# Optimization experiments

Hardware: AMD Instinct MI355X
Metric: run time of the kernel (lower is better)

Reference implementation:

```python
import jax, jax.numpy as jnp
import numpy as np
import math

HIDDEN = 768
HEADS = 12
HEAD_DIM = HIDDEN // HEADS
BLOCK = 256
TOPK = 3
BATCH = 2
SEQ = 2048


def setup_inputs() -> dict:
    key = jax.random.key(0)
    ks = jax.random.split(key, 5)
    s = 1.0 / math.sqrt(HIDDEN)
    return {
        "hidden_states": jax.random.normal(ks[0], (BATCH, SEQ, HIDDEN), jnp.float32),
        "Wq": jax.random.normal(ks[1], (HIDDEN, HIDDEN), jnp.float32) * s,
        "Wk": jax.random.normal(ks[2], (HIDDEN, HIDDEN), jnp.float32) * s,
        "Wv": jax.random.normal(ks[3], (HIDDEN, HIDDEN), jnp.float32) * s,
        "Wo": jax.random.normal(ks[4], (HIDDEN, HIDDEN), jnp.float32) * s,
    }


def _rope(x, sin, cos):
    # x: [B, H, S, D]; rotate-half RoPE
    d2 = x.shape[-1] // 2
    x1, x2 = x[..., :d2], x[..., d2:]
    return x * cos + jnp.concatenate([-x2, x1], axis=-1) * sin


def reference(hidden_states, Wq, Wk, Wv, Wo):
    B, S, Hd = hidden_states.shape
    H, D, bs, K = HEADS, HEAD_DIM, BLOCK, TOPK
    nb = S // bs  # number of key blocks
    scale = 1.0 / math.sqrt(D)

    def split_heads(x):
        return x.reshape(B, S, H, D).transpose(0, 2, 1, 3)  # [B,H,S,D]

    q = split_heads(hidden_states @ Wq.T)
    k = split_heads(hidden_states @ Wk.T)
    v = split_heads(hidden_states @ Wv.T)

    # rotary embedding (standard rotate-half RoPE, base 10000)
    inv_freq = 1.0 / (10000.0 ** (jnp.arange(0, D, 2, dtype=jnp.float32) / D))
    ang = jnp.arange(S, dtype=jnp.float32)[:, None] * inv_freq[None, :]  # [S, D/2]
    emb = jnp.concatenate([ang, ang], axis=-1)  # [S, D]
    sin, cos = jnp.sin(emb), jnp.cos(emb)
    q = _rope(q, sin, cos)
    k = _rope(k, sin, cos)

    # mean-pooled block representations of keys: [B,H,nb,D]
    block_reps = k.reshape(B, H, nb, bs, D).mean(axis=3)

    # routing scores: per-token score against each block rep
    bscores = jnp.einsum('bhsd,bhnd->bhsn', q, block_reps) * scale  # [B,H,S,nb]
    pos = jnp.arange(S)
    cur = pos // bs                       # current block of each query, [S]
    blk = jnp.arange(nb)
    future = blk[None, None, None, :] > cur[None, None, :, None]
    bscores = jnp.where(future, -jnp.inf, bscores)
    # current block is force-selected (score set to dtype max)
    is_cur = blk[None, None, None, :] == cur[None, None, :, None]
    bscores = jnp.where(is_cur, jnp.finfo(bscores.dtype).max, bscores)

    _, topk_idx = jax.lax.top_k(bscores, min(K, nb))  # [B,H,S,K]
    selected = jnp.sum(jax.nn.one_hot(topk_idx, nb, dtype=jnp.float32), axis=-2) > 0  # [B,H,S,nb]

    # per-key-position mask: key t allowed iff its block is selected for query i,
    # and within the current block only t <= i (matches original truncation).
    sel_t = selected[:, :, :, cur]                          # [B,H,Sq,Sk]
    intra_ok = (cur[None, :] != cur[:, None]) | (pos[None, :] <= pos[:, None])  # [Sq,Sk]
    mask = sel_t & intra_ok[None, None]

    scores = jnp.einsum('bhqd,bhkd->bhqk', q, k) * scale
    scores = jnp.where(mask, scores, -jnp.inf)
    probs = jax.nn.softmax(scores, axis=-1)
    out = jnp.einsum('bhqk,bhkd->bhqd', probs, v)

    out = out.transpose(0, 2, 1, 3).reshape(B, S, Hd)
    return out @ Wo.T
```

## Files before the change

kernel.cpp:

```cpp
#include <hip/hip_runtime.h>
#include <math.h>


#define HID   768
#define NH    12
#define DH    64
#define SEQN  2048
#define BATCH 2
#define NTOK  (BATCH*SEQN)
#define NB    8
#define BLKSZ 256
#define NEG_INF (-__builtin_huge_valf())
#define POS_INF (__builtin_huge_valf())
#define LO_SCALE 2048.0f
#define LO_INV   (1.0f/2048.0f)
#define EXP2C    0.18033688f

#define SPLIT_ROWS 1024
#define NBH   (BATCH*NH)

typedef unsigned short u16;
typedef _Float16 v8hf __attribute__((ext_vector_type(8)));
typedef float    v4f  __attribute__((ext_vector_type(4)));

__device__ __forceinline__ u16 f2h(float x) {
    _Float16 h = (_Float16)x;
    return __builtin_bit_cast(u16, h);
}
__device__ __forceinline__ float h2f(u16 u) {
    return (float)__builtin_bit_cast(_Float16, u);
}
__device__ __forceinline__ v8hf ldhf8(const u16* p) {
    return *reinterpret_cast<const v8hf*>(p);
}
__device__ __forceinline__ void g2lds16(const u16* g, u16* l) {
    __builtin_amdgcn_global_load_lds(
        (const __attribute__((address_space(1))) void*)g,
        (__attribute__((address_space(3))) void*)l, 16, 0, 0);
}
#define MFMA16(a, b, c) __builtin_amdgcn_mfma_f32_16x16x32_f16(a, b, c, 0, 0, 0)

__device__ const int g_uord[48] = {
    46,47,44,45,15,
    42,43,40,41,14,
    38,39,36,37,13,
    34,35,32,33,12,
    30,31,28,29,11,
    26,27,24,25,10,
    22,23,20,21, 9,
    18,19,16,17, 8,
     7, 6, 5, 4, 3, 2, 1, 0
};

__global__ __launch_bounds__(256)
void preproc_k(const float* __restrict__ X,  const float* __restrict__ Wq,
               const float* __restrict__ Wk, const float* __restrict__ Wv,
               const float* __restrict__ Wo, float2* __restrict__ tab,
               u16* __restrict__ Xh, u16* __restrict__ Xl,
               u16* __restrict__ Wq2, u16* __restrict__ Wk2,
               u16* __restrict__ Wv2, u16* __restrict__ Wo2)
{
    const int NW = HID * HID;
    const int id = blockIdx.x;
    const int tid = threadIdx.x;
    if (id < 12288) {
        const int i = id * 256 + tid;
        const float x = X[i];
        const u16 h = f2h(x);
        Xh[i] = h;
        Xl[i] = f2h((x - h2f(h)) * LO_SCALE);
    } else if (id < 21504) {
        const int j = (id - 12288) * 256 + tid;
        const int z = j / NW, i = j - z * NW;
        const float* src = (z == 0) ? Wq : (z == 1) ? Wk : (z == 2) ? Wv : Wo;
        u16* dst = (z == 0) ? Wq2 : (z == 1) ? Wk2 : (z == 2) ? Wv2 : Wo2;
        const float x = src[i];
        const u16 h = f2h(x);
        dst[i] = h;
        dst[i + NW] = f2h((x - h2f(h)) * LO_SCALE);
    } else {
        const int i = (id - 21504) * 256 + tid;
        const int s = i >> 5, f = i & 31;
        const double y  = exp((double)f * (log(10000.0) / 32.0));
        const float yf = (float)y;
        const float invf = 1.0f / yf;
        const float ang  = (float)s * invf;
        tab[i] = make_float2((float)sin((double)ang), (float)cos((double)ang));
    }
}

__device__ __forceinline__
void qkv_mainloop(const u16* __restrict__ Ah, const u16* __restrict__ Al,
                  const u16* __restrict__ Bh, const u16* __restrict__ Bl,
                  int m0, int nb0, bool hasC0,
                  u16* As, u16* Bs, v4f acc01[2][4], v4f acc2[2][4])
{
    const int tid = threadIdx.x;
    const int w = tid >> 6, lane = tid & 63;
    const int col = lane & 15, quad = lane >> 4;
    const int AOFF = 128 * 64, BOFF = 64 * 64;

    int a_row[4], a_gl[4];
    #pragma unroll
    for (int r = 0; r < 4; r++) {
        const int g = r * 256 + tid;
        a_row[r] = g >> 3;
        a_gl[r]  = (g & 7) ^ (a_row[r] & 7);
    }
    int b_row[2], b_gl[2];
    #pragma unroll
    for (int r = 0; r < 2; r++) {
        const int g = r * 256 + tid;
        b_row[r] = g >> 3;
        b_gl[r]  = (g & 7) ^ (b_row[r] & 7);
    }

    for (int itc = 0; itc < HID / 64; itc++) {
        const int k0 = itc * 64;
        __syncthreads();
        #pragma unroll
        for (int r = 0; r < 4; r++)
            g2lds16(Ah + (size_t)(m0 + a_row[r]) * HID + k0 + a_gl[r] * 8,
                    &As[(r * 256 + w * 64) * 8]);
        if (hasC0) {
            #pragma unroll
            for (int r = 0; r < 4; r++)
                g2lds16(Al + (size_t)(m0 + a_row[r]) * HID + k0 + a_gl[r] * 8,
                        &As[AOFF + (r * 256 + w * 64) * 8]);
        }
        #pragma unroll
        for (int r = 0; r < 2; r++) {
            g2lds16(Bh + (size_t)(nb0 + b_row[r]) * HID + k0 + b_gl[r] * 8,
                    &Bs[(r * 256 + w * 64) * 8]);
            g2lds16(Bl + (size_t)(nb0 + b_row[r]) * HID + k0 + b_gl[r] * 8,
                    &Bs[BOFF + (r * 256 + w * 64) * 8]);
        }
        __syncthreads();
        #pragma unroll
        for (int ks = 0; ks < 2; ks++) {
            v8hf afh[2], afl[2], bfh[4], bfl[4];
            #pragma unroll
            for (int mt = 0; mt < 2; mt++) {
                const int row = w * 32 + mt * 16 + col;
                const int gph = (ks * 4 + quad) ^ (row & 7);
                afh[mt] = ldhf8(&As[row * 64 + gph * 8]);
                if (hasC0) afl[mt] = ldhf8(&As[AOFF + row * 64 + gph * 8]);
            }
            #pragma unroll
            for (int nt = 0; nt < 4; nt++) {
                const int row = nt * 16 + col;
                const int gph = (ks * 4 + quad) ^ (row & 7);
                bfh[nt] = ldhf8(&Bs[row * 64 + gph * 8]);
                bfl[nt] = ldhf8(&Bs[BOFF + row * 64 + gph * 8]);
            }
            #pragma unroll
            for (int mt = 0; mt < 2; mt++)
                #pragma unroll
                for (int nt = 0; nt < 4; nt++) {
                    if (hasC0)
                        acc01[mt][nt] = MFMA16(afl[mt], bfh[nt], acc01[mt][nt]);
                    acc01[mt][nt] = MFMA16(afh[mt], bfl[nt], acc01[mt][nt]);
                    acc2[mt][nt]  = MFMA16(afh[mt], bfh[nt], acc2[mt][nt]);
                }
        }
    }
    __syncthreads();
}

__global__ __launch_bounds__(256, 3)
void qkv_fused_gemm_k(const u16* __restrict__ Xh, const u16* __restrict__ Xl,
                      const u16* __restrict__ Wq2, const u16* __restrict__ Wk2,
                      const u16* __restrict__ Wv2, const float2* __restrict__ tab,
                      float* __restrict__ q32, u16* __restrict__ kh16,
                      u16* __restrict__ vth, float* __restrict__ partial)
{
    __shared__ u16 As[2 * 128 * 64];
    __shared__ u16 Bs[2 * 64 * 64];
    float (*psum)[64] = (float(*)[64])As;

    const int NW = HID * HID;
    const int id    = blockIdx.x;
    const int xcd   = id & 7, loc = id >> 3;
    const int mtile = xcd * 4 + (loc & 3);
    const int ntile = loc >> 2;
    const int m0  = mtile * 128;
    const int mat = ntile / 12;
    const int nb0 = (ntile - mat * 12) * 64;
    const u16* Bh = (mat == 0) ? Wq2 : (mat == 1) ? Wk2 : Wv2;

    v4f acc01[2][4] = {}, acc2[2][4] = {};
    qkv_mainloop(Xh, Xl, Bh, Bh + NW, m0, nb0, mat != 2, As, Bs, acc01, acc2);

    v4f acc[2][4];
    #pragma unroll
    for (int mt = 0; mt < 2; mt++)
        #pragma unroll
        for (int nt = 0; nt < 4; nt++)
            #pragma unroll
            for (int r = 0; r < 4; r++)
                acc[mt][nt][r] = acc01[mt][nt][r] * LO_INV + acc2[mt][nt][r];

    const int tid = threadIdx.x;
    const int w = tid >> 6, lane = tid & 63;
    const int col = lane & 15, quad = lane >> 4;
    const int b = m0 >> 11;
    const int h = nb0 >> 6;
    const size_t bh = (size_t)b * NH + h;

    if (mat == 2) {
        #pragma unroll
        for (int nt = 0; nt < 4; nt++) {
            const int d = nt * 16 + col;
            #pragma unroll
            for (int mt = 0; mt < 2; mt++) {
                const int m = m0 + w * 32 + mt * 16 + quad * 4;
                const int s = m & (SEQN - 1);
                ushort4 pk = make_ushort4(f2h(acc[mt][nt][0]), f2h(acc[mt][nt][1]),
                                          f2h(acc[mt][nt][2]), f2h(acc[mt][nt][3]));
                *(ushort4*)&vth[(bh * DH + d) * SEQN + s] = pk;
            }
        }
        return;
    }

    float vsum[4] = {0.f, 0.f, 0.f, 0.f};
    #pragma unroll
    for (int mt = 0; mt < 2; mt++) {
        #pragma unroll
        for (int nt = 0; nt < 4; nt++) {
            const int d = nt * 16 + col;
            #pragma unroll
            for (int r = 0; r < 4; r++) {
                const int m = m0 + w * 32 + mt * 16 + quad * 4 + r;
                const int s = m & (SEQN - 1);
                const float part = acc[mt][nt ^ 2][r];
                const float2 sc = tab[(s << 5) + (d & 31)];
                const float val = (d < 32) ? acc[mt][nt][r] * sc.y - part * sc.x
                                           : acc[mt][nt][r] * sc.y + part * sc.x;
                const size_t idx = (bh * SEQN + s) * DH + d;
                if (mat == 0) {
                    q32[idx] = val;
                } else {
                    kh16[idx] = f2h(val);
                    vsum[nt] += val;
                }
            }
        }
    }
    if (mat == 1) {
        #pragma unroll
        for (int nt = 0; nt < 4; nt++) {
            float v = vsum[nt];
            v += __shfl_xor(v, 16);
            v += __shfl_xor(v, 32);
            if (quad == 0) psum[w][nt * 16 + col] = v;
        }
        __syncthreads();
        if (tid < 64) {
            const float s4 = (psum[0][tid] + psum[1][tid])
                           + (psum[2][tid] + psum[3][tid]);
            const int nblk = (m0 & (SEQN - 1)) >> 8;
            const int half = (m0 >> 7) & 1;
            partial[((bh * NB + nblk) * 2 + half) * 64 + tid] = s4;
        }
    }
}

__global__ __launch_bounds__(256, 3)
void out_gemm_mfma_k(const u16* __restrict__ Ah, const u16* __restrict__ Wo2,
                     float* __restrict__ C)
{
    __shared__ u16 As[64 * 64];
    __shared__ u16 Bs[2 * 64 * 64];
    const int BOFF = 64 * 64;

    const int NW = HID * HID;
    const int id    = blockIdx.x;
    const int xcd   = id & 7, loc = id >> 3;
    const int mtile = xcd * 8 + (loc & 7);
    const int ntile = loc >> 3;
    const int m0 = mtile * 64, n0 = ntile * 64;
    const int tid = threadIdx.x;
    const int w = tid >> 6, lane = tid & 63;
    const int col = lane & 15, quad = lane >> 4;

    const int r0 = tid >> 3,         gl0 = (tid & 7) ^ (r0 & 7);
    const int r1 = (256 + tid) >> 3, gl1 = ((256 + tid) & 7) ^ (r1 & 7);

    const u16* Bhp = Wo2;
    const u16* Blp = Wo2 + NW;

    v4f accL[4] = {}, accH[4] = {};
    for (int itc = 0; itc < HID / 64; itc++) {
        const int k0 = itc * 64;
        __syncthreads();
        g2lds16(Ah  + (size_t)(m0 + r0) * HID + k0 + gl0 * 8, &As[(w * 64) * 8]);
        g2lds16(Ah  + (size_t)(m0 + r1) * HID + k0 + gl1 * 8, &As[(256 + w * 64) * 8]);
        g2lds16(Bhp + (size_t)(n0 + r0) * HID + k0 + gl0 * 8, &Bs[(w * 64) * 8]);
        g2lds16(Bhp + (size_t)(n0 + r1) * HID + k0 + gl1 * 8, &Bs[(256 + w * 64) * 8]);
        g2lds16(Blp + (size_t)(n0 + r0) * HID + k0 + gl0 * 8, &Bs[BOFF + (w * 64) * 8]);
        g2lds16(Blp + (size_t)(n0 + r1) * HID + k0 + gl1 * 8, &Bs[BOFF + (256 + w * 64) * 8]);
        __syncthreads();
        #pragma unroll
        for (int ks = 0; ks < 2; ks++) {
            const int arow = w * 16 + col;
            v8hf a = ldhf8(&As[arow * 64 + (((ks * 4 + quad) ^ (arow & 7))) * 8]);
            #pragma unroll
            for (int nt = 0; nt < 4; nt++) {
                const int row = nt * 16 + col;
                const int g = (ks * 4 + quad) ^ (row & 7);
                accH[nt] = MFMA16(a, ldhf8(&Bs[row * 64 + g * 8]), accH[nt]);
                accL[nt] = MFMA16(a, ldhf8(&Bs[BOFF + row * 64 + g * 8]), accL[nt]);
            }
        }
    }

    #pragma unroll
    for (int nt = 0; nt < 4; nt++)
        #pragma unroll
        for (int r = 0; r < 4; r++) {
            const int m = m0 + w * 16 + quad * 4 + r;
            C[(size_t)m * HID + n0 + nt * 16 + col] =
                accL[nt][r] * LO_INV + accH[nt][r];
        }
}

__global__ __launch_bounds__(64)
void reps_reduce_k(const float* __restrict__ partial, float* __restrict__ reps)
{
    const int bhn = blockIdx.x;
    const int d = threadIdx.x;
    const float* p = &partial[(size_t)bhn * 128 + d];
    double s = (double)p[0] + (double)p[64];
    reps[(size_t)bhn * 64 + d] = (float)(s * (1.0 / 256.0));
}

__global__ __launch_bounds__(128)
void select_topk_k(const float* __restrict__ qg, const float* __restrict__ reps,
                   unsigned* __restrict__ selm)
{
    __shared__ float rs[NB][DH];
    const int bh = blockIdx.y;
    const int tid = threadIdx.x;
    for (int idx = tid; idx < NB * DH; idx += 128)
        rs[idx >> 6][idx & 63] = reps[(size_t)bh * NB * DH + idx];
    __syncthreads();

    const int qq = blockIdx.x * 128 + tid;
    const float* qv = &qg[((size_t)bh * SEQN + qq) * DH];
    float qr[DH];
    #pragma unroll
    for (int c = 0; c < 16; c++) {
        float4 t = *(const float4*)&qv[c * 4];
        qr[c*4+0]=t.x; qr[c*4+1]=t.y; qr[c*4+2]=t.z; qr[c*4+3]=t.w;
    }
    const int cur = qq >> 8;
    double sc[NB];
    #pragma unroll
    for (int n = 0; n < NB; n++) {
        double ssum = 0.0;
        for (int d = 0; d < DH; d++) ssum += (double)qr[d] * (double)rs[n][d];
        sc[n] = ssum * 0.125;
    }
    for (int n = cur + 1; n < NB; n++) sc[n] = -1e300;
    sc[cur] = 1e300;
    unsigned mask = 0;
    for (int p = 0; p < 3; p++) {
        int bi = -1; double bv = 0.0;
        for (int n = 0; n < NB; n++) {
            if ((mask >> n) & 1) continue;
            if (bi < 0 || sc[n] > bv) { bi = n; bv = sc[n]; }
        }
        mask |= 1u << bi;
    }
    selm[(size_t)bh * SEQN + qq] = mask;
}

__global__ __launch_bounds__(256, 4)
void moba_attn_k(const float* __restrict__ q32, const u16* __restrict__ kh16,
                 const u16* __restrict__ vth, const unsigned* __restrict__ selm,
                 u16* __restrict__ aoh, float* __restrict__ po,
                 float* __restrict__ ml)
{
    __shared__ u16 kbuf[2][64 * 64];
    __shared__ u16 vbuf[2][64 * 64];
    __shared__ u16 plds[4][16][64];
    unsigned* s_uni = (unsigned*)&vbuf[1][0];

    const int id  = blockIdx.x;
    const int xcd = id & 7, loc = id >> 3;
    const int bh  = xcd * 3 + loc / 48;
    const int u   = g_uord[loc % 48];
    int qb, split, stride;
    if (u < 16) { qb = u;                 split = 0;          stride = 1; }
    else        { qb = 16 + ((u - 16) >> 1); split = (u - 16) & 1; stride = 2; }
    const int q0  = qb * 64;
    const int cur = q0 >> 8;
    const int tid = threadIdx.x;
    const int wave = tid >> 6, lane = tid & 63;
    const int col = lane & 15, quad = lane >> 4;
    const int qw0 = q0 + wave * 16;
    const int qpos = qw0 + col;
    const size_t bhS = (size_t)bh * SEQN;
    const size_t bhV = (size_t)bh * DH;

    if (tid == 0) *s_uni = 0;
    __syncthreads();
    const unsigned mymask = selm[bhS + qw0 + col];
    unsigned uw = mymask;
    #pragma unroll
    for (int off = 1; off < 16; off <<= 1) uw |= __shfl_xor(uw, off);
    if (lane == 0) atomicOr(s_uni, uw);
    const unsigned wmask = __builtin_amdgcn_readfirstlane(uw);

    v8hf qh[2], ql[2];
    #pragma unroll
    for (int ks = 0; ks < 2; ks++) {
        const float* qp = &q32[(bhS + qw0 + col) * DH + ks * 32 + quad * 8];
        float4 f0 = *(const float4*)qp;
        float4 f1 = *(const float4*)(qp + 4);
        float qf[8] = {f0.x, f0.y, f0.z, f0.w, f1.x, f1.y, f1.z, f1.w};
        union { u16 u[8]; v8hf h; } uh, ul;
        #pragma unroll
        for (int j = 0; j < 8; j++) {
            u16 hb = f2h(qf[j]);
            uh.u[j] = hb;
            ul.u[j] = f2h((qf[j] - h2f(hb)) * LO_SCALE);
        }
        qh[ks] = uh.h; ql[ks] = ul.h;
    }
    __syncthreads();
    const unsigned uni = __builtin_amdgcn_readfirstlane(*s_uni);

    int n_nxt = __builtin_ctz(uni), c_nxt = 0;
    bool has_nxt = true;
    auto c2max = [&](int n) { return (n == cur) ? ((q0 + 63 - n * BLKSZ) >> 6) : 3; };
    auto advance1 = [&]() {
        if (c_nxt < c2max(n_nxt)) { c_nxt++; return; }
        for (int nn = n_nxt + 1; nn < NB; nn++)
            if ((uni >> nn) & 1) { n_nxt = nn; c_nxt = 0; return; }
        has_nxt = false;
    };
    for (int i = 0; i < split; i++) if (has_nxt) advance1();
    int n_cur = n_nxt, c_cur = c_nxt;
    const bool cur_valid = has_nxt;

    const size_t srow0 = (size_t)bh * SPLIT_ROWS + (q0 - SPLIT_ROWS);

    if (!cur_valid) {
        if (stride == 2) {
            if (quad == 0) {
                const size_t r = srow0 + wave * 16 + col;
                ml[(r * 2 + split) * 2 + 0] = NEG_INF;
                ml[(r * 2 + split) * 2 + 1] = 0.f;
            }
            #pragma unroll
            for (int nt = 0; nt < 4; nt++)
                #pragma unroll
                for (int r = 0; r < 4; r++) {
                    const size_t rq = srow0 + wave * 16 + quad * 4 + r;
                    po[(rq * 2 + split) * 64 + nt * 16 + col] = 0.f;
                }
        }
        return;
    }
    for (int i = 0; i < stride; i++) if (has_nxt) advance1();

    const int sg_row0 = tid >> 3;
    const int sg_gl0  = (tid & 7) ^ (sg_row0 & 7);
    const int sg_row1 = (256 + tid) >> 3;
    const int sg_gl1  = ((256 + tid) & 7) ^ (sg_row1 & 7);
    auto stage = [&](int n, int c2, int buf) {
        const int kb = n * BLKSZ + c2 * 64;
        u16* kd = (u16*)kbuf[buf];
        u16* vd = (u16*)vbuf[buf];
        const size_t ks0 = (bhS + kb + sg_row0) * DH + sg_gl0 * 8;
        const size_t ks1 = (bhS + kb + sg_row1) * DH + sg_gl1 * 8;
        const size_t vs0 = (bhV + sg_row0) * SEQN + kb + sg_gl0 * 8;
        const size_t vs1 = (bhV + sg_row1) * SEQN + kb + sg_gl1 * 8;
        g2lds16(kh16 + ks0, kd + (wave * 64) * 8);
        g2lds16(kh16 + ks1, kd + (256 + wave * 64) * 8);
        g2lds16(vth + vs0, vd + (wave * 64) * 8);
        g2lds16(vth + vs1, vd + (256 + wave * 64) * 8);
    };

    const v4f zero4 = {0.f, 0.f, 0.f, 0.f};
    v4f oacc[4] = {zero4, zero4, zero4, zero4};
    float m_i = NEG_INF, l_i = 0.f;
    const int psw = (col & 7) << 1;

    stage(n_cur, c_cur, 0);
    int t = 0;
    while (true) {
        __syncthreads();
        if (has_nxt) stage(n_nxt, c_nxt, (t + 1) & 1);

        const int n  = n_cur;
        const int kb = n * BLKSZ + c_cur * 64;
        const bool iscur = (n == cur);
        const float selinf = ((mymask >> n) & 1) ? 0.f : POS_INF;
        const bool need_mask = iscur && (kb + 63 > qw0);
        const u16* kd = (const u16*)kbuf[t & 1];
        const u16* vd = (const u16*)vbuf[t & 1];

        if ((wmask >> n) & 1) {
            v4f sf[4];
            __builtin_amdgcn_s_setprio(1);
            #pragma unroll
            for (int mt = 0; mt < 4; mt++) {
                const int row = mt * 16 + col;
                const int r7 = row & 7;
                v8hf kh0 = ldhf8(&kd[(row * 8 + (quad ^ r7)) * 8]);
                v8hf kh1 = ldhf8(&kd[(row * 8 + ((4 + quad) ^ r7)) * 8]);
                v4f c = zero4;
                c = MFMA16(kh0, ql[0], c);
                c = MFMA16(kh1, ql[1], c);
                #pragma unroll
                for (int r = 0; r < 4; r++) c[r] *= LO_INV;
                c = MFMA16(kh0, qh[0], c);
                c = MFMA16(kh1, qh[1], c);
                sf[mt] = c;
            }
            __builtin_amdgcn_s_setprio(0);

            if (need_mask) {
                #pragma unroll
                for (int mt = 0; mt < 4; mt++)
                    #pragma unroll
                    for (int r = 0; r < 4; r++) {
                        const int kidx = kb + mt * 16 + quad * 4 + r;
                        sf[mt][r] = (kidx <= qpos) ? sf[mt][r] : NEG_INF;
                    }
            }

            float rm = NEG_INF;
            #pragma unroll
            for (int mt = 0; mt < 4; mt++)
                #pragma unroll
                for (int r = 0; r < 4; r++) rm = fmaxf(rm, sf[mt][r]);
            rm = fmaxf(rm, __shfl_xor(rm, 16));
            rm = fmaxf(rm, __shfl_xor(rm, 32));
            rm = rm - selinf;
            const float mnew  = fmaxf(m_i, rm);
            const float alpha = (m_i == NEG_INF) ? 0.f : exp2f((m_i - mnew) * EXP2C);
            const float biasC = ((mnew == NEG_INF) ? 0.f : mnew * EXP2C) + selinf;

            float lsum = 0.f;
            #pragma unroll
            for (int mt = 0; mt < 4; mt++) {
                ushort4 hv;
                #pragma unroll
                for (int r = 0; r < 4; r++) {
                    float p = exp2f(fmaf(sf[mt][r], EXP2C, -biasC));
                    lsum += p;
                    u16 hu = f2h(p);
                    if (r == 0) hv.x = hu;
                    else if (r == 1) hv.y = hu;
                    else if (r == 2) hv.z = hu;
                    else hv.w = hu;
                }
                *(ushort4*)&plds[wave][col][((mt * 4 + quad) ^ psw) * 4] = hv;
            }
            lsum += __shfl_xor(lsum, 16);
            lsum += __shfl_xor(lsum, 32);
            l_i = l_i * alpha + lsum;
            m_i = mnew;

            float ar[4];
            #pragma unroll
            for (int r = 0; r < 4; r++) ar[r] = __shfl(alpha, quad * 4 + r, 16);
            #pragma unroll
            for (int nt = 0; nt < 4; nt++)
                #pragma unroll
                for (int r = 0; r < 4; r++) oacc[nt][r] *= ar[r];

            __threadfence_block();

            __builtin_amdgcn_s_setprio(1);
            #pragma unroll
            for (int ks2 = 0; ks2 < 2; ks2++) {
                v8hf ph = ldhf8(&plds[wave][col][((ks2 * 8 + quad * 2) ^ psw) * 4]);
                #pragma unroll
                for (int nt = 0; nt < 4; nt++) {
                    const int row = nt * 16 + col;
                    const int g = (ks2 * 4 + quad) ^ (row & 7);
                    v8hf vh = ldhf8(&vd[(row * 8 + g) * 8]);
                    oacc[nt] = MFMA16(ph, vh, oacc[nt]);
                }
            }
            __builtin_amdgcn_s_setprio(0);
        }

        if (!has_nxt) break;
        n_cur = n_nxt; c_cur = c_nxt;
        for (int i = 0; i < stride; i++) if (has_nxt) advance1();
        t++;
    }

    if (stride == 2) {
        if (quad == 0) {
            const size_t r = srow0 + wave * 16 + col;
            ml[(r * 2 + split) * 2 + 0] = m_i;
            ml[(r * 2 + split) * 2 + 1] = l_i;
        }
        #pragma unroll
        for (int nt = 0; nt < 4; nt++)
            #pragma unroll
            for (int r = 0; r < 4; r++) {
                const size_t rq = srow0 + wave * 16 + quad * 4 + r;
                po[(rq * 2 + split) * 64 + nt * 16 + col] = oacc[nt][r];
            }
        return;
    }

    const int b = bh / NH, h = bh % NH;
    const float invl = 1.f / l_i;
    float ir[4];
    #pragma unroll
    for (int r = 0; r < 4; r++) ir[r] = __shfl(invl, quad * 4 + r, 16);
    #pragma unroll
    for (int nt = 0; nt < 4; nt++)
        #pragma unroll
        for (int r = 0; r < 4; r++) {
            const int qi = qw0 + quad * 4 + r;
            const size_t idx = ((size_t)b * SEQN + qi) * HID + h * DH + nt * 16 + col;
            aoh[idx] = f2h(oacc[nt][r] * ir[r]);
        }
}

__global__ __launch_bounds__(256)
void attn_combine_k(const float* __restrict__ po, const float* __restrict__ ml,
                    u16* __restrict__ aoh)
{
    const int g = blockIdx.x * 256 + threadIdx.x;
    const int d = g & 63;
    const size_t row = (size_t)(g >> 6);
    const int bh = (int)(row >> 10);
    const int qlocal = (int)(row & 1023);
    const float m0 = ml[(row * 2 + 0) * 2 + 0], l0 = ml[(row * 2 + 0) * 2 + 1];
    const float m1 = ml[(row * 2 + 1) * 2 + 0], l1 = ml[(row * 2 + 1) * 2 + 1];
    const float m  = fmaxf(m0, m1);
    const float a0 = (m0 == NEG_INF) ? 0.f : exp2f((m0 - m) * EXP2C);
    const float a1 = (m1 == NEG_INF) ? 0.f : exp2f((m1 - m) * EXP2C);
    const float o  = po[(row * 2 + 0) * 64 + d] * a0
                   + po[(row * 2 + 1) * 64 + d] * a1;
    const float inv = 1.f / (l0 * a0 + l1 * a1);
    const int b = bh / NH, h = bh % NH;
    const int q = SPLIT_ROWS + qlocal;
    aoh[((size_t)b * SEQN + q) * HID + h * DH + d] = f2h(o * inv);
}

extern "C" void kernel_launch(void* const* d_in, const int* in_sizes, int n_in,
                              void* d_out, int out_size, void* d_ws, size_t ws_size,
                              hipStream_t stream)
{
    const float* X  = (const float*)d_in[0];
    const float* Wq = (const float*)d_in[1];
    const float* Wk = (const float*)d_in[2];
    const float* Wv = (const float*)d_in[3];
    const float* Wo = (const float*)d_in[4];
    float* out = (float*)d_out;

    char* p = (char*)d_ws;
    float* q32 = (float*)p;                p += (size_t)NTOK*HID*4;
    u16* kh16 = (u16*)p;                   p += (size_t)NTOK*HID*2;
    u16* vth  = (u16*)p;                   p += (size_t)NTOK*HID*2;
    u16* Xh   = (u16*)p;                   p += (size_t)NTOK*HID*2;
    u16* Xl   = (u16*)p;                   p += (size_t)NTOK*HID*2;
    u16* Wq2  = (u16*)p;                   p += (size_t)HID*HID*2*2;
    u16* Wk2  = (u16*)p;                   p += (size_t)HID*HID*2*2;
    u16* Wv2  = (u16*)p;                   p += (size_t)HID*HID*2*2;
    u16* Wo2  = (u16*)p;                   p += (size_t)HID*HID*2*2;
    float* partial = (float*)p;            p += (size_t)BATCH*NH*NB*2*64*4;
    float* reps    = (float*)p;            p += (size_t)BATCH*NH*NB*DH*4;
    unsigned* selm = (unsigned*)p;         p += (size_t)BATCH*NH*SEQN*4;
    float2* tab    = (float2*)p;           p += (size_t)SEQN*32*8;
    u16* aoh = Xh;

    float* po = (float*)Xl;
    float* ml = po + (size_t)NBH * SPLIT_ROWS * 2 * 64;

    preproc_k<<<dim3(21760), 256, 0, stream>>>(X, Wq, Wk, Wv, Wo, tab,
                                               Xh, Xl, Wq2, Wk2, Wv2, Wo2);

    qkv_fused_gemm_k<<<dim3(1152), 256, 0, stream>>>(
        Xh, Xl, Wq2, Wk2, Wv2, tab, q32, kh16, vth, partial);

    reps_reduce_k<<<dim3(BATCH*NH*NB), 64, 0, stream>>>(partial, reps);
    select_topk_k<<<dim3(SEQN/128, BATCH*NH), 128, 0, stream>>>(q32, reps, selm);

    moba_attn_k<<<dim3(1152), 256, 0, stream>>>(
        q32, kh16, vth, selm, aoh, po, ml);

    attn_combine_k<<<dim3(6144), 256, 0, stream>>>(po, ml, aoh);

    out_gemm_mfma_k<<<dim3(768), 256, 0, stream>>>(aoh, Wo2, out);
}
```

Before: 214.3 us.

## Vectorize preprocessing and single-buffer V in attention for higher occupancy

The preprocessing kernel now handles four floats per thread with float4 loads and ushort4 stores, and launches a quarter as many blocks. In the attention kernel the V tile is single-buffered and loaded after the K/QK phase starts, which cuts LDS per block so the launch bound can ask for 5 blocks per CU. This adds an extra block-wide barrier per iteration between the softmax and PV phases. V load latency is now less hidden because V is fetched only for the current tile.

Measured after the change: 215.8 us. No clear change (+0.7%).

```diff
diff --git a/kernel.cpp b/kernel.cpp
--- a/kernel.cpp
+++ b/kernel.cpp
@@ -63,23 +63,39 @@
     const int NW = HID * HID;
     const int id = blockIdx.x;
     const int tid = threadIdx.x;
-    if (id < 12288) {
-        const int i = id * 256 + tid;
-        const float x = X[i];
-        const u16 h = f2h(x);
-        Xh[i] = h;
-        Xl[i] = f2h((x - h2f(h)) * LO_SCALE);
-    } else if (id < 21504) {
-        const int j = (id - 12288) * 256 + tid;
-        const int z = j / NW, i = j - z * NW;
+    if (id < 3072) {
+        const int i = (id * 256 + tid) * 4;
+        const float4 x4 = *(const float4*)&X[i];
+        const float xf[4] = {x4.x, x4.y, x4.z, x4.w};
+        ushort4 h4, l4;
+        u16* hp = (u16*)&h4; u16* lp = (u16*)&l4;
+        #pragma unroll
+        for (int j = 0; j < 4; j++) {
+            const u16 h = f2h(xf[j]);
+            hp[j] = h;
+            lp[j] = f2h((xf[j] - h2f(h)) * LO_SCALE);
+        }
+        *(ushort4*)&Xh[i] = h4;
+        *(ushort4*)&Xl[i] = l4;
+    } else if (id < 5376) {
+        const int j4 = ((id - 3072) * 256 + tid) * 4;
+        const int z = j4 / NW, i = j4 - z * NW;
         const float* src = (z == 0) ? Wq : (z == 1) ? Wk : (z == 2) ? Wv : Wo;
         u16* dst = (z == 0) ? Wq2 : (z == 1) ? Wk2 : (z == 2) ? Wv2 : Wo2;
-        const float x = src[i];
-        const u16 h = f2h(x);
-        dst[i] = h;
-        dst[i + NW] = f2h((x - h2f(h)) * LO_SCALE);
+        const float4 x4 = *(const float4*)&src[i];
+        const float xf[4] = {x4.x, x4.y, x4.z, x4.w};
+        ushort4 h4, l4;
+        u16* hp = (u16*)&h4; u16* lp = (u16*)&l4;
+        #pragma unroll
+        for (int j = 0; j < 4; j++) {
+            const u16 h = f2h(xf[j]);
+            hp[j] = h;
+            lp[j] = f2h((xf[j] - h2f(h)) * LO_SCALE);
+        }
+        *(ushort4*)&dst[i] = h4;
+        *(ushort4*)&dst[i + NW] = l4;
     } else {
-        const int i = (id - 21504) * 256 + tid;
+        const int i = (id - 5376) * 256 + tid;
         const int s = i >> 5, f = i & 31;
         const double y  = exp((double)f * (log(10000.0) / 32.0));
         const float yf = (float)y;
@@ -376,16 +392,16 @@
     selm[(size_t)bh * SEQN + qq] = mask;
 }
 
-__global__ __launch_bounds__(256, 4)
+__global__ __launch_bounds__(256, 5)
 void moba_attn_k(const float* __restrict__ q32, const u16* __restrict__ kh16,
                  const u16* __restrict__ vth, const unsigned* __restrict__ selm,
                  u16* __restrict__ aoh, float* __restrict__ po,
                  float* __restrict__ ml)
 {
     __shared__ u16 kbuf[2][64 * 64];
-    __shared__ u16 vbuf[2][64 * 64];
+    __shared__ u16 vbuf[64 * 64];
     __shared__ u16 plds[4][16][64];
-    unsigned* s_uni = (unsigned*)&vbuf[1][0];
+    unsigned* s_uni = (unsigned*)&plds[0][0][0];
 
     const int id  = blockIdx.x;
     const int xcd = id & 7, loc = id >> 3;
@@ -427,7 +443,7 @@
             uh.u[j] = hb;
             ul.u[j] = f2h((qf[j] - h2f(hb)) * LO_SCALE);
         }
-        qh[ks] = uh.h; ql[ks] = ul.h;
+        qh[ks] = uh.h; ul.h = ul.h; ql[ks] = ul.h;
     }
     __syncthreads();
     const unsigned uni = __builtin_amdgcn_readfirstlane(*s_uni);
@@ -470,18 +486,17 @@
     const int sg_gl0  = (tid & 7) ^ (sg_row0 & 7);
     const int sg_row1 = (256 + tid) >> 3;
     const int sg_gl1  = ((256 + tid) & 7) ^ (sg_row1 & 7);
-    auto stage = [&](int n, int c2, int buf) {
+    auto stage_k = [&](int n, int c2, int buf) {
         const int kb = n * BLKSZ + c2 * 64;
         u16* kd = (u16*)kbuf[buf];
-        u16* vd = (u16*)vbuf[buf];
-        const size_t ks0 = (bhS + kb + sg_row0) * DH + sg_gl0 * 8;
-        const size_t ks1 = (bhS + kb + sg_row1) * DH + sg_gl1 * 8;
-        const size_t vs0 = (bhV + sg_row0) * SEQN + kb + sg_gl0 * 8;
-        const size_t vs1 = (bhV + sg_row1) * SEQN + kb + sg_gl1 * 8;
-        g2lds16(kh16 + ks0, kd + (wave * 64) * 8);
-        g2lds16(kh16 + ks1, kd + (256 + wave * 64) * 8);
-        g2lds16(vth + vs0, vd + (wave * 64) * 8);
-        g2lds16(vth + vs1, vd + (256 + wave * 64) * 8);
+        g2lds16(kh16 + (bhS + kb + sg_row0) * DH + sg_gl0 * 8, kd + (wave * 64) * 8);
+        g2lds16(kh16 + (bhS + kb + sg_row1) * DH + sg_gl1 * 8, kd + (256 + wave * 64) * 8);
+    };
+    auto stage_v = [&](int n, int c2) {
+        const int kb = n * BLKSZ + c2 * 64;
+        u16* vd = (u16*)vbuf;
+        g2lds16(vth + (bhV + sg_row0) * SEQN + kb + sg_gl0 * 8, vd + (wave * 64) * 8);
+        g2lds16(vth + (bhV + sg_row1) * SEQN + kb + sg_gl1 * 8, vd + (256 + wave * 64) * 8);
     };
 
     const v4f zero4 = {0.f, 0.f, 0.f, 0.f};
@@ -489,11 +504,12 @@
     float m_i = NEG_INF, l_i = 0.f;
     const int psw = (col & 7) << 1;
 
-    stage(n_cur, c_cur, 0);
+    stage_k(n_cur, c_cur, 0);
     int t = 0;
     while (true) {
         __syncthreads();
-        if (has_nxt) stage(n_nxt, c_nxt, (t + 1) & 1);
+        stage_v(n_cur, c_cur);
+        if (has_nxt) stage_k(n_nxt, c_nxt, (t + 1) & 1);
 
         const int n  = n_cur;
         const int kb = n * BLKSZ + c_cur * 64;
@@ -501,9 +517,9 @@
         const float selinf = ((mymask >> n) & 1) ? 0.f : POS_INF;
         const bool need_mask = iscur && (kb + 63 > qw0);
         const u16* kd = (const u16*)kbuf[t & 1];
-        const u16* vd = (const u16*)vbuf[t & 1];
-
-        if ((wmask >> n) & 1) {
+
+        const bool act = (wmask >> n) & 1;
+        if (act) {
             v4f sf[4];
             __builtin_amdgcn_s_setprio(1);
             #pragma unroll
@@ -573,9 +589,12 @@
             for (int nt = 0; nt < 4; nt++)
                 #pragma unroll
                 for (int r = 0; r < 4; r++) oacc[nt][r] *= ar[r];
-
-            __threadfence_block();
-
+        }
+
+        __syncthreads();
+
+        if (act) {
+            const u16* vd = (const u16*)vbuf;
             __builtin_amdgcn_s_setprio(1);
             #pragma unroll
             for (int ks2 = 0; ks2 < 2; ks2++) {
@@ -680,8 +699,8 @@
     float* po = (float*)Xl;
     float* ml = po + (size_t)NBH * SPLIT_ROWS * 2 * 64;
 
-    preproc_k<<<dim3(21760), 256, 0, stream>>>(X, Wq, Wk, Wv, Wo, tab,
-                                               Xh, Xl, Wq2, Wk2, Wv2, Wo2);
+    preproc_k<<<dim3(5632), 256, 0, stream>>>(X, Wq, Wk, Wv, Wo, tab,
+                                              Xh, Xl, Wq2, Wk2, Wv2, Wo2);
 
     qkv_fused_gemm_k<<<dim3(1152), 256, 0, stream>>>(
         Xh, Xl, Wq2, Wk2, Wv2, tab, q32, kh16, vth, partial);
```
